# Optimization experiments

Hardware: AMD Instinct MI355X
Metric: run time of the kernel (lower is better)

Reference implementation:

```python
import math
import jax, jax.numpy as jnp
import numpy as np

HEADS = 8
D = 128            # model_dim
PE = D // 2        # position_embedding_size (query_positional_score=True)
MAXP = 32          # max_position_embeddings
LN_EPS = 1e-5


def setup_inputs() -> dict:
    key = jax.random.key(0)
    ks = jax.random.split(key, 7)
    bs, h, w = 8, 32, 32
    hidden_state = jax.random.normal(ks[0], (bs, h, w, D), dtype=jnp.float32)
    row_emb = jax.random.normal(ks[1], (2 * MAXP - 1, PE), dtype=jnp.float32) * 0.02
    col_emb = jax.random.normal(ks[2], (2 * MAXP - 1, PE), dtype=jnp.float32) * 0.02
    # torch Linear weights are (out_features, in_features)
    Wq = jax.random.normal(ks[3], (HEADS * D, D), dtype=jnp.float32) / math.sqrt(D)
    Wk = jax.random.normal(ks[4], (HEADS * D, D), dtype=jnp.float32) / math.sqrt(D)
    Wv = jax.random.normal(ks[5], (D, HEADS * D), dtype=jnp.float32) / math.sqrt(HEADS * D)
    bv = jnp.zeros((D,), dtype=jnp.float32)
    ln_g = jnp.ones((D,), dtype=jnp.float32)
    ln_b = jnp.zeros((D,), dtype=jnp.float32)
    return {"hidden_state": hidden_state, "row_emb": row_emb, "col_emb": col_emb,
            "Wq": Wq, "Wk": Wk, "Wv": Wv, "bv": bv, "ln_g": ln_g, "ln_b": ln_b}


def _layer_norm(x, g, b):
    mu = jnp.mean(x, axis=-1, keepdims=True)
    var = jnp.var(x, axis=-1, keepdims=True)
    return (x - mu) * jax.lax.rsqrt(var + LN_EPS) * g + b


def _forward(hidden_state, row_emb, col_emb, Wq, Wk, Wv, bv, ln_g, ln_b):
    bs, h, w, _ = hidden_state.shape
    x = _layer_norm(hidden_state, ln_g, ln_b)  # pre_norm=True
    sqrt_norm = math.sqrt(D)

    # relative indices (static, h == w == 32 here)
    deltas = np.arange(MAXP)[None, :] - np.arange(MAXP)[:, None]
    rel = deltas + MAXP - 1
    row_embeds = row_emb[rel[:w, :w]]  # (w, w, PE)
    col_embeds = col_emb[rel[:h, :h]]  # (h, h, PE)

    # projections; original does .view(bs, w, h, heads, D) on a (bs,h,w,heads*D) tensor
    q = jnp.einsum('bhwc,oc->bhwo', x, Wq).reshape(bs, w, h, HEADS, D)
    k = jnp.einsum('bhwc,oc->bhwo', x, Wk).reshape(bs, w, h, HEADS, D)

    q_row = q[..., :PE]
    q_col = q[..., PE:]
    row_scores = jnp.einsum('bijhd,ikd->bijhk', q_row, row_embeds)
    col_scores = jnp.einsum('bijhd,jld->bijhl', q_col, col_embeds)
    scores = (row_scores[..., :, None] + col_scores[..., None, :]) / sqrt_norm  # bijhkl
    scores = scores.transpose(0, 2, 1, 3, 5, 4)

    content = jnp.einsum('bijhd,bklhd->bijhkl', q, k) / sqrt_norm
    scores = scores + content.transpose(0, 2, 1, 3, 5, 4)  # (bs, h, w, heads, h, w)

    attn_shape = scores.shape
    probs = jax.nn.softmax(scores.reshape(*attn_shape[:-2], -1), axis=-1).reshape(attn_shape)

    # dropout omitted (inference / p=0)
    context = jnp.einsum('bijhkl,bkld->bijhd', probs, x)
    context = context.reshape(bs, h, w, HEADS * D)
    output = jnp.einsum('bhwc,oc->bhwo', context, Wv) + bv + x
    return output, probs


def reference(hidden_state, row_emb, col_emb, Wq, Wk, Wv, bv, ln_g, ln_b):
    return _forward(hidden_state, row_emb, col_emb, Wq, Wk, Wv, bv, ln_g, ln_b)
```

## Files before the change

kernel.cpp:

```cpp
#include <hip/hip_runtime.h>
#include <hip/hip_bf16.h>

#define HEADS 8
#define D 128
#define QSCALE 0.12751743f
#define PPITCH 2064

typedef unsigned short u16;
typedef unsigned int u32;
typedef __attribute__((ext_vector_type(8))) short short8;
typedef __attribute__((ext_vector_type(4))) float f32x4;

static __device__ inline float sbf2f(short s) {
    return __uint_as_float(((u32)(unsigned short)s) << 16);
}
static __device__ inline u16 f2bf(float f) {
    u32 u = __float_as_uint(f);
    return (u16)((u + 0x7FFFu + ((u >> 16) & 1u)) >> 16);
}
static __device__ inline u32 pk2bf(float a, float b) {
    return (u32)f2bf(a) | ((u32)f2bf(b) << 16);
}
static __device__ inline u32 cvtpk(float a, float b) {
    union { __hip_bfloat162 h; u32 u; } x;
    x.h = __float22bfloat162_rn(make_float2(a, b));
    return x.u;
}
static __device__ inline f32x4 mfma16(short8 a, short8 b, f32x4 c) {
    return __builtin_amdgcn_mfma_f32_16x16x32_bf16(a, b, c, 0, 0, 0);
}
static __device__ inline short8 cvt8(const float* e) {
    f32x4 v0 = *(const f32x4*)e;
    f32x4 v1 = *(const f32x4*)(e + 4);
    union { uint4 u; short8 s; } x;
    x.u = make_uint4(pk2bf(v0[0], v0[1]), pk2bf(v0[2], v0[3]),
                     pk2bf(v1[0], v1[1]), pk2bf(v1[2], v1[3]));
    return x.s;
}

__global__ __launch_bounds__(256) void k_wcvt(const float* __restrict__ Wq,
    const float* __restrict__ Wk, const float* __restrict__ Wv,
    u16* __restrict__ wqk, u16* __restrict__ wv)
{
    int idx = (blockIdx.x * 256 + threadIdx.x) * 4;
    const float* src;
    u16* dst;
    if (idx < 131072)      { src = Wq + idx;           dst = wqk + idx; }
    else if (idx < 262144) { src = Wk + (idx - 131072); dst = wqk + idx; }
    else                   { src = Wv + (idx - 262144); dst = wv + (idx - 262144); }
    f32x4 v = *(const f32x4*)src;
    *(uint2*)dst = make_uint2(pk2bf(v[0], v[1]), pk2bf(v[2], v[3]));
}

__global__ __launch_bounds__(256) void k_lnxt(const float* __restrict__ hs,
    const float* __restrict__ g, const float* __restrict__ bb,
    float* __restrict__ xf, u16* __restrict__ xbf, u16* __restrict__ xt)
{
    __shared__ __align__(16) u16 tl[128][136];
    int b = blockIdx.x, ch = blockIdx.y;
    int tid = threadIdx.x;
    int c4 = (tid & 31) * 4;
    f32x4 g4 = *(const f32x4*)(g + c4);
    f32x4 b4 = *(const f32x4*)(bb + c4);
    const float* src = hs + ((size_t)b * 1024 + ch * 128) * 128;
    #pragma unroll
    for (int it = 0; it < 16; ++it) {
        int p = (tid >> 5) + it * 8;
        f32x4 v = *(const f32x4*)(src + (size_t)p * 128 + c4);
        float s1 = (v[0] + v[1]) + (v[2] + v[3]);
        float s2 = (v[0] * v[0] + v[1] * v[1]) + (v[2] * v[2] + v[3] * v[3]);
        #pragma unroll
        for (int off = 1; off < 32; off <<= 1) {
            s1 += __shfl_xor(s1, off);
            s2 += __shfl_xor(s2, off);
        }
        float mu  = s1 * 0.0078125f;
        float var = s2 * 0.0078125f - mu * mu;
        float inv = rsqrtf(var + 1e-5f);
        f32x4 o;
        #pragma unroll
        for (int q = 0; q < 4; ++q) o[q] = (v[q] - mu) * inv * g4[q] + b4[q];
        size_t row = (size_t)b * 1024 + ch * 128 + p;
        *(f32x4*)(xf + row * 128 + c4) = o;
        *(uint2*)(xbf + row * 128 + c4) = make_uint2(pk2bf(o[0], o[1]), pk2bf(o[2], o[3]));
        tl[c4 + 0][p] = f2bf(o[0]);
        tl[c4 + 1][p] = f2bf(o[1]);
        tl[c4 + 2][p] = f2bf(o[2]);
        tl[c4 + 3][p] = f2bf(o[3]);
    }
    __syncthreads();
    u16* dst = xt + (size_t)b * 131072 + ch * 128;
    #pragma unroll
    for (int i = 0; i < 8; ++i) {
        int d = (tid >> 4) + i * 16, c8 = (tid & 15) * 8;
        *(uint4*)(dst + (size_t)d * 1024 + c8) = *(const uint4*)&tl[d][c8];
    }
}

__global__ __launch_bounds__(256) void k_proj(const u16* __restrict__ xbf,
    const u16* __restrict__ wqk,
    u16* __restrict__ q_bf, u16* __restrict__ kt_bf)
{
    int tid = threadIdx.x;
    int w = tid >> 6, l = tid & 63, h = l >> 4, ln = l & 15;
    int t0 = blockIdx.x * 64 + w * 16;
    int o0 = blockIdx.y * 64;
    short8 a[4];
    #pragma unroll
    for (int s = 0; s < 4; ++s)
        a[s] = *(const short8*)(xbf + (size_t)(t0 + ln) * 128 + s * 32 + h * 8);
    f32x4 acc[4];
    #pragma unroll
    for (int n = 0; n < 4; ++n) acc[n] = f32x4{0.f, 0.f, 0.f, 0.f};
    #pragma unroll
    for (int n = 0; n < 4; ++n) {
        const u16* wsrc = wqk + (size_t)(o0 + n * 16 + ln) * 128;
        #pragma unroll
        for (int s = 0; s < 4; ++s) {
            short8 bf = *(const short8*)(wsrc + s * 32 + h * 8);
            acc[n] = mfma16(a[s], bf, acc[n]);
        }
    }
    bool isq = (o0 < 1024);
    float oscale = isq ? QSCALE : 1.0f;
    int head = (o0 & 1023) >> 7;
    int od_base = (o0 & 127);
    u16* basep = isq ? q_bf : kt_bf;
    #pragma unroll
    for (int n = 0; n < 4; ++n) {
        int d0 = od_base + n * 16 + ln;
        #pragma unroll
        for (int r = 0; r < 4; ++r) {
            int t = t0 + h * 4 + r;
            int b = t >> 10, pos = t & 1023;
            size_t row;
            if (isq) row = (size_t)(b * 8 + head) * 1024 + pos;
            else { int I = pos >> 5, J = pos & 31; row = (size_t)(b * 8 + head) * 1024 + (J * 32 + I); }
            basep[row * 128 + d0] = f2bf(acc[n][r] * oscale);
        }
    }
}

__global__ __launch_bounds__(256) void k_bias(const u16* __restrict__ q_bf,
    const float* __restrict__ row_emb, const float* __restrict__ col_emb,
    float* __restrict__ rbias, float* __restrict__ cbias)
{
    __shared__ __align__(16) float cbf[32][68];
    int tid = threadIdx.x;
    int w = tid >> 6, l = tid & 63, h = l >> 4, ln = l & 15;
    int blk = blockIdx.x;
    int bh = blk >> 5, I = blk & 31;
    const u16* qb = q_bf + ((size_t)bh * 1024 + I * 32) * 128;
    size_t obase = (size_t)blk * 1024;
    if (w < 2) {
        short8 a0 = *(const short8*)(qb + (size_t)(w * 16 + ln) * 128 + h * 8);
        short8 a1 = *(const short8*)(qb + (size_t)(w * 16 + ln) * 128 + 32 + h * 8);
        f32x4 o[2] = {f32x4{0,0,0,0}, f32x4{0,0,0,0}};
        #pragma unroll
        for (int n = 0; n < 2; ++n) {
            int K = n * 16 + ln;
            const float* e = row_emb + (size_t)(K - I + 31) * 64 + h * 8;
            o[n] = mfma16(a0, cvt8(e), o[n]);
            o[n] = mfma16(a1, cvt8(e + 32), o[n]);
        }
        #pragma unroll
        for (int n = 0; n < 2; ++n)
            #pragma unroll
            for (int r = 0; r < 4; ++r)
                rbias[obase + (size_t)(w * 16 + h * 4 + r) * 32 + n * 16 + ln] = o[n][r];
    } else {
        int m = w - 2;
        short8 a0 = *(const short8*)(qb + (size_t)(m * 16 + ln) * 128 + 64 + h * 8);
        short8 a1 = *(const short8*)(qb + (size_t)(m * 16 + ln) * 128 + 96 + h * 8);
        f32x4 o[4] = {f32x4{0,0,0,0}, f32x4{0,0,0,0}, f32x4{0,0,0,0}, f32x4{0,0,0,0}};
        #pragma unroll
        for (int n = 0; n < 4; ++n) {
            int p = n * 16 + ln;
            if (p > 62) p = 62;
            const float* e = col_emb + (size_t)p * 64 + h * 8;
            o[n] = mfma16(a0, cvt8(e), o[n]);
            o[n] = mfma16(a1, cvt8(e + 32), o[n]);
        }
        #pragma unroll
        for (int n = 0; n < 4; ++n)
            #pragma unroll
            for (int r = 0; r < 4; ++r)
                cbf[m * 16 + h * 4 + r][n * 16 + ln] = o[n][r];
    }
    __syncthreads();
    int J = tid >> 3, L0 = (tid & 7) * 4;
    float4 g;
    g.x = cbf[J][L0 + 0 - J + 31];
    g.y = cbf[J][L0 + 1 - J + 31];
    g.z = cbf[J][L0 + 2 - J + 31];
    g.w = cbf[J][L0 + 3 - J + 31];
    *(float4*)(cbias + obase + (size_t)J * 32 + L0) = g;
}

__global__ __launch_bounds__(512, 4) void k_attn(const u16* __restrict__ q_bf,
    const u16* __restrict__ kt_bf, const u16* __restrict__ xt_bf,
    const float* __restrict__ rbias, const float* __restrict__ cbias,
    float* __restrict__ probs, u16* __restrict__ ctx_bf)
{
    __shared__ __align__(16) char P[32 * PPITCH];
    __shared__ float wred[256];

    int tid = threadIdx.x;
    int w = tid >> 6, l = tid & 63, h = l >> 4, ln = l & 15;
    int flat = blockIdx.x;
    int bh = flat >> 5, I = flat & 31;
    int b = bh >> 3, head = bh & 7;
    int kk0 = w * 128;

    const float* rbase = rbias + (size_t)(bh * 32 + I) * 1024;
    const float* cbase = cbias + (size_t)(bh * 32 + I) * 1024;
    f32x4 rbr[2][2], cbr[2];
    #pragma unroll
    for (int n = 0; n < 2; ++n) {
        int J = n * 16 + ln;
        rbr[n][0] = *(const f32x4*)(rbase + J * 32 + h * 4);
        rbr[n][1] = *(const f32x4*)(rbase + J * 32 + 16 + h * 4);
        cbr[n]    = *(const f32x4*)(cbase + J * 32 + w * 4);
    }

    f32x4 acc[2][8];
    #pragma unroll
    for (int n = 0; n < 2; ++n)
        #pragma unroll
        for (int t = 0; t < 8; ++t) acc[n][t] = f32x4{0.f, 0.f, 0.f, 0.f};
    const u16* kbase = kt_bf + ((size_t)bh * 1024 + kk0) * 128;
    const u16* qbase = q_bf + ((size_t)bh * 1024 + I * 32) * 128;
    #pragma unroll
    for (int s = 0; s < 4; ++s) {
        short8 q0 = *(const short8*)(qbase + (size_t)ln * 128 + s * 32 + h * 8);
        short8 q1 = *(const short8*)(qbase + (size_t)(16 + ln) * 128 + s * 32 + h * 8);
        #pragma unroll
        for (int t = 0; t < 8; ++t) {
            short8 kf = *(const short8*)(kbase + (size_t)(t * 16 + ln) * 128 + s * 32 + h * 8);
            acc[0][t] = mfma16(kf, q0, acc[0][t]);
            acc[1][t] = mfma16(kf, q1, acc[1][t]);
        }
    }

    #pragma unroll
    for (int n = 0; n < 2; ++n) {
        int J = n * 16 + ln;
        float sum = 0.f;
        #pragma unroll
        for (int t = 0; t < 8; ++t) {
            float cbv = cbr[n][t >> 1];
            float p0 = exp2f(acc[n][t][0] + rbr[n][t & 1][0] + cbv);
            float p1 = exp2f(acc[n][t][1] + rbr[n][t & 1][1] + cbv);
            float p2 = exp2f(acc[n][t][2] + rbr[n][t & 1][2] + cbv);
            float p3 = exp2f(acc[n][t][3] + rbr[n][t & 1][3] + cbv);
            sum += (p0 + p1) + (p2 + p3);
            *(uint2*)(P + J * PPITCH + (kk0 + t * 16 + h * 4) * 2) =
                make_uint2(cvtpk(p0, p1), cvtpk(p2, p3));
        }
        sum += __shfl_xor(sum, 16);
        sum += __shfl_xor(sum, 32);
        if (l < 16) wred[w * 32 + J] = sum;
    }
    __syncthreads();

    f32x4 sum0 = f32x4{0.f, 0.f, 0.f, 0.f};
    f32x4 sum1 = f32x4{0.f, 0.f, 0.f, 0.f};
    #pragma unroll
    for (int w2 = 0; w2 < 8; ++w2) {
        sum0 += *(const f32x4*)&wred[w2 * 32 + h * 4];
        sum1 += *(const f32x4*)&wred[w2 * 32 + 16 + h * 4];
    }
    int j = tid >> 4;
    float sd = 0.f;
    #pragma unroll
    for (int w2 = 0; w2 < 8; ++w2) sd += wred[w2 * 32 + j];
    float invd = 1.0f / sd;

    {
        float* prow = probs + ((((size_t)(b * 32 + j) * 32 + I) * 8 + head) << 10);
        #pragma unroll
        for (int i = 0; i < 8; ++i) {
            int kk = i * 128 + (tid & 15) * 8;
            short8 pv = *(const short8*)(P + j * PPITCH + kk * 2);
            float4 o0, o1;
            o0.x = sbf2f(pv[0]) * invd; o0.y = sbf2f(pv[1]) * invd;
            o0.z = sbf2f(pv[2]) * invd; o0.w = sbf2f(pv[3]) * invd;
            o1.x = sbf2f(pv[4]) * invd; o1.y = sbf2f(pv[5]) * invd;
            o1.z = sbf2f(pv[6]) * invd; o1.w = sbf2f(pv[7]) * invd;
            *(float4*)(prow + kk)     = o0;
            *(float4*)(prow + kk + 4) = o1;
        }
    }

    f32x4 cacc[2] = {f32x4{0,0,0,0}, f32x4{0,0,0,0}};
    int d0 = w * 16;
    const u16* xb = xt_bf + (size_t)b * 131072 + (size_t)(d0 + ln) * 1024 + h * 8;
    #pragma unroll
    for (int ks = 0; ks < 32; ++ks) {
        short8 xf8 = *(const short8*)(xb + ks * 32);
        #pragma unroll
        for (int m = 0; m < 2; ++m) {
            short8 pa = *(const short8*)(P + (m * 16 + ln) * PPITCH + (ks * 32 + h * 8) * 2);
            cacc[m] = mfma16(pa, xf8, cacc[m]);
        }
    }
    #pragma unroll
    for (int m = 0; m < 2; ++m)
        #pragma unroll
        for (int r = 0; r < 4; ++r) {
            int J = m * 16 + h * 4 + r;
            float inv = 1.0f / (m ? sum1[r] : sum0[r]);
            ctx_bf[((size_t)(b * 32 + J) * 32 + I) * 1024 + head * 128 + d0 + ln] =
                f2bf(cacc[m][r] * inv);
        }
}

__global__ __launch_bounds__(256) void k_out(const u16* __restrict__ ctx_bf,
    const u16* __restrict__ wv_bf, const float* __restrict__ bv,
    const float* __restrict__ xf, float* __restrict__ out)
{
    int tid = threadIdx.x;
    int w = tid >> 6, l = tid & 63, h = l >> 4, ln = l & 15;
    int wm = w >> 1, wn = w & 1;
    int t0 = blockIdx.x * 32 + wm * 16;
    int o0 = blockIdx.y * 64 + wn * 32;
    f32x4 acc[2] = {f32x4{0,0,0,0}, f32x4{0,0,0,0}};
    for (int ks = 0; ks < 32; ++ks) {
        short8 a = *(const short8*)(ctx_bf + (size_t)(t0 + ln) * 1024 + ks * 32 + h * 8);
        #pragma unroll
        for (int nt = 0; nt < 2; ++nt) {
            short8 bb = *(const short8*)(wv_bf + (size_t)(o0 + nt * 16 + ln) * 1024 + ks * 32 + h * 8);
            acc[nt] = mfma16(a, bb, acc[nt]);
        }
    }
    #pragma unroll
    for (int nt = 0; nt < 2; ++nt) {
        int o = o0 + nt * 16 + ln;
        float bvv = bv[o];
        #pragma unroll
        for (int r = 0; r < 4; ++r) {
            int t = t0 + h * 4 + r;
            out[(size_t)t * 128 + o] = acc[nt][r] + bvv + xf[(size_t)t * 128 + o];
        }
    }
}

extern "C" void kernel_launch(void* const* d_in, const int* in_sizes, int n_in,
                              void* d_out, int out_size, void* d_ws, size_t ws_size,
                              hipStream_t stream) {
    (void)in_sizes; (void)n_in; (void)out_size; (void)ws_size;
    const float* hs      = (const float*)d_in[0];
    const float* row_emb = (const float*)d_in[1];
    const float* col_emb = (const float*)d_in[2];
    const float* Wq      = (const float*)d_in[3];
    const float* Wk      = (const float*)d_in[4];
    const float* Wv      = (const float*)d_in[5];
    const float* bv      = (const float*)d_in[6];
    const float* ln_g    = (const float*)d_in[7];
    const float* ln_b    = (const float*)d_in[8];

    float* out   = (float*)d_out;
    float* probs = out + 1048576;

    char* ws = (char*)d_ws;
    float* xf     = (float*)(ws);
    u16*   xbf    = (u16*)(ws + 4194304);
    u16*   q_bf   = (u16*)(ws + 6291456);
    u16*   kt_bf  = (u16*)(ws + 23068672);
    u16*   xt     = (u16*)(ws + 39845888);
    u16*   wqk_bf = (u16*)(ws + 41943040);
    u16*   wv_bf  = (u16*)(ws + 42467328);
    u16*   ctx    = (u16*)(ws + 42729472);
    float* rbias  = (float*)(ws + 59506688);
    float* cbias  = (float*)(ws + 67895296);

    k_wcvt <<<384, 256, 0, stream>>>(Wq, Wk, Wv, wqk_bf, wv_bf);
    k_lnxt <<<dim3(8, 8), 256, 0, stream>>>(hs, ln_g, ln_b, xf, xbf, xt);
    k_proj <<<dim3(128, 32), 256, 0, stream>>>(xbf, wqk_bf, q_bf, kt_bf);
    k_bias <<<2048, 256, 0, stream>>>(q_bf, row_emb, col_emb, rbias, cbias);
    k_attn <<<2048, 512, 0, stream>>>(q_bf, kt_bf, xt, rbias, cbias, probs, ctx);
    k_out  <<<dim3(256, 2), 256, 0, stream>>>(ctx, wv_bf, bv, xf, out);
}
```

Before: 277.3 us.

## Stage K tiles into LDS via async global_load_lds with double buffering

The QK^T phase of the attention kernel now streams each wave's K slice through LDS in 4KB chunks using global_load_lds, double-buffered with explicit vmcnt waits, instead of loading K fragments directly from global memory. Q fragments are hoisted into registers before the loop. The probability tile reuses the same LDS region with an XOR swizzle instead of a padded pitch. The aim is to overlap K fetches with MFMA work and avoid LDS bank conflicts. The cost is more hand-written synchronisation and a tighter dependence on the swizzle and waitcnt logic being correct.

```diff
diff --git a/kernel.cpp b/kernel.cpp
--- a/kernel.cpp
+++ b/kernel.cpp
@@ -4,7 +4,6 @@
 #define HEADS 8
 #define D 128
 #define QSCALE 0.12751743f
-#define PPITCH 2064
 
 typedef unsigned short u16;
 typedef unsigned int u32;
@@ -36,6 +35,12 @@
     x.u = make_uint4(pk2bf(v0[0], v0[1]), pk2bf(v0[2], v0[3]),
                      pk2bf(v1[0], v1[1]), pk2bf(v1[2], v1[3]));
     return x.s;
+}
+static __device__ __forceinline__ void gload_lds16(const void* g, void* l) {
+    __builtin_amdgcn_global_load_lds(
+        (const __attribute__((address_space(1))) u32*)g,
+        (__attribute__((address_space(3))) u32*)(u32)(uintptr_t)l,
+        16, 0, 0);
 }
 
 __global__ __launch_bounds__(256) void k_wcvt(const float* __restrict__ Wq,
@@ -202,7 +207,7 @@
     const float* __restrict__ rbias, const float* __restrict__ cbias,
     float* __restrict__ probs, u16* __restrict__ ctx_bf)
 {
-    __shared__ __align__(16) char P[32 * PPITCH];
+    __shared__ __align__(16) char KT[8 * 8192];
     __shared__ float wred[256];
 
     int tid = threadIdx.x;
@@ -211,6 +216,8 @@
     int bh = flat >> 5, I = flat & 31;
     int b = bh >> 3, head = bh & 7;
     int kk0 = w * 128;
+    char* reg = KT + w * 8192;
+    const char* ktg = (const char*)(kt_bf + ((size_t)bh * 1024 + kk0) * 128);
 
     const float* rbase = rbias + (size_t)(bh * 32 + I) * 1024;
     const float* cbase = cbias + (size_t)(bh * 32 + I) * 1024;
@@ -222,23 +229,49 @@
         rbr[n][1] = *(const f32x4*)(rbase + J * 32 + 16 + h * 4);
         cbr[n]    = *(const f32x4*)(cbase + J * 32 + w * 4);
     }
+    const u16* qbase = q_bf + ((size_t)bh * 1024 + I * 32) * 128;
+    short8 q0[4], q1[4];
+    #pragma unroll
+    for (int s = 0; s < 4; ++s) {
+        q0[s] = *(const short8*)(qbase + (size_t)ln * 128 + s * 32 + h * 8);
+        q1[s] = *(const short8*)(qbase + (size_t)(16 + ln) * 128 + s * 32 + h * 8);
+    }
+
+    auto stage_chunk = [&](int c, int buf) {
+        const char* gs = ktg + c * 4096;
+        char* ld = reg + buf * 4096;
+        #pragma unroll
+        for (int i = 0; i < 4; ++i) {
+            int key = ((i * 4 + (l >> 4)) & 7) << 4;
+            int o = i * 1024 + l * 16;
+            gload_lds16(gs + (o ^ key), ld + i * 1024);
+        }
+    };
+    stage_chunk(0, 0);
+    stage_chunk(1, 1);
 
     f32x4 acc[2][8];
     #pragma unroll
     for (int n = 0; n < 2; ++n)
         #pragma unroll
         for (int t = 0; t < 8; ++t) acc[n][t] = f32x4{0.f, 0.f, 0.f, 0.f};
-    const u16* kbase = kt_bf + ((size_t)bh * 1024 + kk0) * 128;
-    const u16* qbase = q_bf + ((size_t)bh * 1024 + I * 32) * 128;
-    #pragma unroll
-    for (int s = 0; s < 4; ++s) {
-        short8 q0 = *(const short8*)(qbase + (size_t)ln * 128 + s * 32 + h * 8);
-        short8 q1 = *(const short8*)(qbase + (size_t)(16 + ln) * 128 + s * 32 + h * 8);
-        #pragma unroll
-        for (int t = 0; t < 8; ++t) {
-            short8 kf = *(const short8*)(kbase + (size_t)(t * 16 + ln) * 128 + s * 32 + h * 8);
-            acc[0][t] = mfma16(kf, q0, acc[0][t]);
-            acc[1][t] = mfma16(kf, q1, acc[1][t]);
+    int xk = (ln & 7) << 4;
+    #pragma unroll
+    for (int c = 0; c < 8; ++c) {
+        if (c < 7) asm volatile("s_waitcnt vmcnt(4)" ::: "memory");
+        else       asm volatile("s_waitcnt vmcnt(0)" ::: "memory");
+        const char* cb = reg + (c & 1) * 4096;
+        short8 kf[4];
+        #pragma unroll
+        for (int s = 0; s < 4; ++s)
+            kf[s] = *(const short8*)(cb + ((ln * 256 + s * 64 + h * 16) ^ xk));
+        asm volatile("s_waitcnt lgkmcnt(0)" ::: "memory");
+        __builtin_amdgcn_sched_barrier(0);
+        if (c + 2 < 8) stage_chunk(c + 2, c & 1);
+        #pragma unroll
+        for (int s = 0; s < 4; ++s) {
+            acc[0][c] = mfma16(kf[s], q0[s], acc[0][c]);
+            acc[1][c] = mfma16(kf[s], q1[s], acc[1][c]);
         }
     }
 
@@ -253,8 +286,9 @@
             float p1 = exp2f(acc[n][t][1] + rbr[n][t & 1][1] + cbv);
             float p2 = exp2f(acc[n][t][2] + rbr[n][t & 1][2] + cbv);
             float p3 = exp2f(acc[n][t][3] + rbr[n][t & 1][3] + cbv);
+            acc[n][t] = f32x4{p0, p1, p2, p3};
             sum += (p0 + p1) + (p2 + p3);
-            *(uint2*)(P + J * PPITCH + (kk0 + t * 16 + h * 4) * 2) =
+            *(uint2*)(reg + ((J * 256 + t * 32 + h * 8) ^ xk)) =
                 make_uint2(cvtpk(p0, p1), cvtpk(p2, p3));
         }
         sum += __shfl_xor(sum, 16);
@@ -278,10 +312,12 @@
 
     {
         float* prow = probs + ((((size_t)(b * 32 + j) * 32 + I) * 8 + head) << 10);
+        int jx = (j & 7) << 4;
         #pragma unroll
         for (int i = 0; i < 8; ++i) {
             int kk = i * 128 + (tid & 15) * 8;
-            short8 pv = *(const short8*)(P + j * PPITCH + kk * 2);
+            short8 pv = *(const short8*)(KT + i * 8192 +
+                            ((j * 256 + (tid & 15) * 16) ^ jx));
             float4 o0, o1;
             o0.x = sbf2f(pv[0]) * invd; o0.y = sbf2f(pv[1]) * invd;
             o0.z = sbf2f(pv[2]) * invd; o0.w = sbf2f(pv[3]) * invd;
@@ -300,7 +336,8 @@
         short8 xf8 = *(const short8*)(xb + ks * 32);
         #pragma unroll
         for (int m = 0; m < 2; ++m) {
-            short8 pa = *(const short8*)(P + (m * 16 + ln) * PPITCH + (ks * 32 + h * 8) * 2);
+            short8 pa = *(const short8*)(KT + (ks >> 2) * 8192 +
+                (((m * 16 + ln) * 256 + (ks & 3) * 64 + h * 16) ^ xk));
             cacc[m] = mfma16(pa, xf8, cacc[m]);
         }
     }
```

New measurement: 248.7 us. 1.12x faster.
